# Optimization experiments

Hardware: AMD Instinct MI355X
Metric: run time of the kernel (lower is better)

The kernel has to match this reference:

```python
import jax, jax.numpy as jnp
import numpy as np
import math

NEG_BIG = -1e9

def setup_inputs() -> dict:
    key = jax.random.key(0)
    k1, k2, k3 = jax.random.split(key, 3)
    N, C, T = 16, 64, 2048
    qkv = jax.random.normal(k1, (N, 3 * C, T), dtype=jnp.float32)
    pos = jax.random.normal(k2, (N, C, T), dtype=jnp.float32)
    attn_mask = jax.random.randint(k3, (N, T, T), 0, 2) == 1  # bool mask, True = masked
    return {"qkv": qkv, "pos": pos, "attn_mask": attn_mask}

def reference(qkv, pos, attn_mask):
    ch = qkv.shape[1] // 3
    q, k, v = jnp.split(qkv, 3, axis=1)  # each [N, C, T]
    q = q + pos
    k = k + pos
    v = v + pos
    scale = 1.0 / math.sqrt(math.sqrt(ch))
    # [N, T, T] attention logits
    weight = jnp.einsum('bct,bcs->bts', q * scale, k * scale)
    weight = jnp.where(attn_mask, NEG_BIG, weight)
    weight = jax.nn.softmax(weight.astype(jnp.float32), axis=-1).astype(weight.dtype)
    return jnp.einsum('bts,bcs->bct', weight, v)
```

## Files before the change

### kernel.cpp

```cpp
#include <hip/hip_runtime.h>
#include <hip/hip_bf16.h>

typedef float f32x4 __attribute__((ext_vector_type(4)));
typedef unsigned int u32x4 __attribute__((ext_vector_type(4)));
typedef short s16x8 __attribute__((ext_vector_type(8)));

#define L2E 1.44269504088896340736f

static __device__ __forceinline__ unsigned int bf16_rne(float f) {
    unsigned int u = __builtin_bit_cast(unsigned int, f);
    return (u + 0x7fffu + ((u >> 16) & 1u)) >> 16;
}
static __device__ __forceinline__ unsigned int pack_bf16x2(float lo, float hi) {
    return bf16_rne(lo) | (bf16_rne(hi) << 16);
}
static __device__ __forceinline__ unsigned int cvt_pk_bf16(float lo, float hi) {
    unsigned int r;
    asm("v_cvt_pk_bf16_f32 %0, %1, %2" : "=v"(r) : "v"(lo), "v"(hi));
    return r;
}

__global__ __launch_bounds__(256) void qkv_prep(const float* __restrict__ qkv,
                                                const float* __restrict__ pos,
                                                unsigned short* __restrict__ qs,
                                                unsigned short* __restrict__ kt,
                                                unsigned short* __restrict__ vt)
{
    __shared__ unsigned short QtS[64][72];
    __shared__ unsigned short KtS[64][72];
    const int b    = blockIdx.y;
    const int t0   = blockIdx.x * 64;
    const int i    = threadIdx.x;
    const int crow = i >> 2;
    const int t16  = (i & 3) * 16;
    const float QSCALE = 0.125f * L2E;

    float pr[16];
    {
        const f32x4* pp = reinterpret_cast<const f32x4*>(
            pos + ((size_t)(b * 64 + crow)) * 2048 + t0 + t16);
        #pragma unroll
        for (int j = 0; j < 4; ++j) {
            f32x4 v = __builtin_nontemporal_load(pp + j);
            pr[4*j+0] = v[0]; pr[4*j+1] = v[1]; pr[4*j+2] = v[2]; pr[4*j+3] = v[3];
        }
    }
    const float* qp = qkv + ((size_t)(b * 192 + crow)) * 2048 + t0 + t16;
    {
        #pragma unroll
        for (int j = 0; j < 4; ++j) {
            f32x4 v = __builtin_nontemporal_load(reinterpret_cast<const f32x4*>(qp) + j);
            #pragma unroll
            for (int e = 0; e < 4; ++e)
                QtS[t16 + 4*j + e][crow] =
                    (unsigned short)bf16_rne((v[e] + pr[4*j+e]) * QSCALE);
        }
    }
    {
        const float* kp = qp + (size_t)64 * 2048;
        #pragma unroll
        for (int j = 0; j < 4; ++j) {
            f32x4 v = __builtin_nontemporal_load(reinterpret_cast<const f32x4*>(kp) + j);
            #pragma unroll
            for (int e = 0; e < 4; ++e)
                KtS[t16 + 4*j + e][crow] =
                    (unsigned short)bf16_rne(v[e] + pr[4*j+e]);
        }
    }
    {
        const float* vp = qp + (size_t)128 * 2048;
        unsigned int vv[8];
        #pragma unroll
        for (int j = 0; j < 4; ++j) {
            f32x4 v = __builtin_nontemporal_load(reinterpret_cast<const f32x4*>(vp) + j);
            vv[2*j+0] = pack_bf16x2(v[0] + pr[4*j+0], v[1] + pr[4*j+1]);
            vv[2*j+1] = pack_bf16x2(v[2] + pr[4*j+2], v[3] + pr[4*j+3]);
        }
        unsigned short* dst = vt + ((size_t)(b * 64 + crow)) * 2048 + t0 + t16;
        reinterpret_cast<u32x4*>(dst)[0] = (u32x4){vv[0], vv[1], vv[2], vv[3]};
        reinterpret_cast<u32x4*>(dst)[1] = (u32x4){vv[4], vv[5], vv[6], vv[7]};
    }
    __syncthreads();
    {
        const int trow = i >> 2;
        const int c16  = (i & 3) * 16;
        u32x4 a0 = *reinterpret_cast<const u32x4*>(&QtS[trow][c16]);
        u32x4 a1 = *reinterpret_cast<const u32x4*>(&QtS[trow][c16 + 8]);
        unsigned short* qd = qs + ((size_t)(b * 2048 + t0 + trow)) * 64 + c16;
        reinterpret_cast<u32x4*>(qd)[0] = a0;
        reinterpret_cast<u32x4*>(qd)[1] = a1;
        u32x4 b0 = *reinterpret_cast<const u32x4*>(&KtS[trow][c16]);
        u32x4 b1 = *reinterpret_cast<const u32x4*>(&KtS[trow][c16 + 8]);
        unsigned short* kd = kt + ((size_t)(b * 2048 + t0 + trow)) * 64 + c16;
        reinterpret_cast<u32x4*>(kd)[0] = b0;
        reinterpret_cast<u32x4*>(kd)[1] = b1;
    }
}

__global__ __launch_bounds__(256) void attn_kernel(const unsigned short* __restrict__ qs,
                                                   const unsigned short* __restrict__ kt,
                                                   const unsigned short* __restrict__ vt,
                                                   const void* __restrict__ maskp,
                                                   float* __restrict__ out)
{
    __shared__ unsigned short Klds[2][64][72];
    __shared__ unsigned short Vlds[2][64][72];

    const int b    = blockIdx.y;
    const int t0   = blockIdx.x * 64;
    const int tid  = threadIdx.x;
    const int wave = tid >> 6;
    const int lane = tid & 63;
    const int ln   = lane & 15;
    const int lg   = lane >> 4;

    unsigned int accm = 0;
    {
        const unsigned int* mu = (const unsigned int*)maskp;
        #pragma unroll
        for (int j = 0; j < 16; ++j) accm |= mu[j];
    }
    const bool maskIsBool = (accm & 0xffffff00u) != 0u;

    const int tg = t0 + 16 * wave + ln;
    s16x8 qf[2];
    #pragma unroll
    for (int kc = 0; kc < 2; ++kc)
        qf[kc] = *reinterpret_cast<const s16x8*>(
            qs + ((size_t)(b * 2048 + tg)) * 64 + 32 * kc + 8 * lg);

    f32x4 acc[4];
    #pragma unroll
    for (int n = 0; n < 4; ++n) acc[n] = (f32x4){0.f, 0.f, 0.f, 0.f};
    float M = -3.0e38f, L = 0.0f;

    const int stRow = tid >> 2;
    const int stC16 = (tid & 3) * 16;
    const unsigned short* kbase = kt + ((size_t)(b * 2048 + stRow)) * 64 + stC16;
    const unsigned short* vbase = vt + ((size_t)(b * 64 + stRow)) * 2048 + stC16;
    const size_t mrowoff = ((size_t)b * 2048 + (size_t)tg) * 2048;

    unsigned int m_cur[4];

    {
        u32x4 ka0 = reinterpret_cast<const u32x4*>(kbase)[0];
        u32x4 ka1 = reinterpret_cast<const u32x4*>(kbase)[1];
        u32x4 va0 = reinterpret_cast<const u32x4*>(vbase)[0];
        u32x4 va1 = reinterpret_cast<const u32x4*>(vbase)[1];
        if (maskIsBool) {
            const unsigned char* mp = (const unsigned char*)maskp + mrowoff + 4 * lg;
            #pragma unroll
            for (int ti = 0; ti < 4; ++ti)
                m_cur[ti] = __builtin_nontemporal_load(
                    reinterpret_cast<const unsigned int*>(mp + 16 * ti));
        } else {
            const u32x4* mp = reinterpret_cast<const u32x4*>(
                (const unsigned int*)maskp + mrowoff + 4 * lg);
            #pragma unroll
            for (int ti = 0; ti < 4; ++ti) {
                u32x4 x = __builtin_nontemporal_load(mp + 4 * ti);
                m_cur[ti] = (x[0] ? 1u : 0u) | ((x[1] ? 1u : 0u) << 8) |
                            ((x[2] ? 1u : 0u) << 16) | ((x[3] ? 1u : 0u) << 24);
            }
        }
        *reinterpret_cast<u32x4*>(&Klds[0][stRow][stC16])     = ka0;
        *reinterpret_cast<u32x4*>(&Klds[0][stRow][stC16 + 8]) = ka1;
        *reinterpret_cast<u32x4*>(&Vlds[0][stRow][stC16])     = va0;
        *reinterpret_cast<u32x4*>(&Vlds[0][stRow][stC16 + 8]) = va1;
    }
    __syncthreads();

    int cur = 0;
    for (int st = 0; st < 32; ++st) {
        u32x4 ka0, ka1, va0, va1;
        unsigned int m_nxt[4];
        const bool pf = (st < 31);
        if (pf) {
            const int s1 = (st + 1) * 64;
            const unsigned short* ks = kbase + (size_t)s1 * 64;
            const unsigned short* vs = vbase + s1;
            ka0 = reinterpret_cast<const u32x4*>(ks)[0];
            ka1 = reinterpret_cast<const u32x4*>(ks)[1];
            va0 = reinterpret_cast<const u32x4*>(vs)[0];
            va1 = reinterpret_cast<const u32x4*>(vs)[1];
            if (maskIsBool) {
                const unsigned char* mp = (const unsigned char*)maskp + mrowoff + s1 + 4 * lg;
                #pragma unroll
                for (int ti = 0; ti < 4; ++ti)
                    m_nxt[ti] = __builtin_nontemporal_load(
                        reinterpret_cast<const unsigned int*>(mp + 16 * ti));
            } else {
                const u32x4* mp = reinterpret_cast<const u32x4*>(
                    (const unsigned int*)maskp + mrowoff + s1 + 4 * lg);
                #pragma unroll
                for (int ti = 0; ti < 4; ++ti) {
                    u32x4 x = __builtin_nontemporal_load(mp + 4 * ti);
                    m_nxt[ti] = (x[0] ? 1u : 0u) | ((x[1] ? 1u : 0u) << 8) |
                                ((x[2] ? 1u : 0u) << 16) | ((x[3] ? 1u : 0u) << 24);
                }
            }
        }

        f32x4 S[4];
        #pragma unroll
        for (int ti = 0; ti < 4; ++ti) S[ti] = (f32x4){0.f, 0.f, 0.f, 0.f};
        __builtin_amdgcn_s_setprio(1);
        #pragma unroll
        for (int kc = 0; kc < 2; ++kc) {
            #pragma unroll
            for (int ti = 0; ti < 4; ++ti) {
                s16x8 kf = *reinterpret_cast<const s16x8*>(
                    &Klds[cur][16 * ti + ln][32 * kc + 8 * lg]);
                S[ti] = __builtin_amdgcn_mfma_f32_16x16x32_bf16(kf, qf[kc], S[ti], 0, 0, 0);
            }
        }
        __builtin_amdgcn_s_setprio(0);

        float p[4][4];
        #pragma unroll
        for (int ti = 0; ti < 4; ++ti) {
            #pragma unroll
            for (int r = 0; r < 4; ++r)
                p[ti][r] = ((m_cur[ti] >> (8 * r)) & 0xffu) ? -1e9f : S[ti][r];
        }
        float tm = fmaxf(fmaxf(fmaxf(p[0][0], p[0][1]), fmaxf(p[0][2], p[0][3])),
                         fmaxf(fmaxf(p[1][0], p[1][1]), fmaxf(p[1][2], p[1][3])));
        tm = fmaxf(tm, fmaxf(fmaxf(fmaxf(p[2][0], p[2][1]), fmaxf(p[2][2], p[2][3])),
                             fmaxf(fmaxf(p[3][0], p[3][1]), fmaxf(p[3][2], p[3][3]))));
        tm = fmaxf(tm, __shfl_xor(tm, 16, 64));
        tm = fmaxf(tm, __shfl_xor(tm, 32, 64));
        if (!__all(tm <= M)) {
            const float Mn    = fmaxf(M, tm);
            const float alpha = exp2f(M - Mn);
            L *= alpha;
            #pragma unroll
            for (int n = 0; n < 4; ++n) acc[n] *= alpha;
            M = Mn;
        }
        float tsum = 0.f;
        #pragma unroll
        for (int ti = 0; ti < 4; ++ti)
            #pragma unroll
            for (int r = 0; r < 4; ++r) {
                p[ti][r] = exp2f(p[ti][r] - M);
                tsum += p[ti][r];
            }
        tsum += __shfl_xor(tsum, 16, 64);
        tsum += __shfl_xor(tsum, 32, 64);
        L += tsum;

        unsigned int pk[4][2];
        #pragma unroll
        for (int ti = 0; ti < 4; ++ti) {
            pk[ti][0] = cvt_pk_bf16(p[ti][0], p[ti][1]);
            pk[ti][1] = cvt_pk_bf16(p[ti][2], p[ti][3]);
        }
        unsigned int pfr[2][4];
        #pragma unroll
        for (int kc2 = 0; kc2 < 2; ++kc2)
            #pragma unroll
            for (int a2 = 0; a2 < 2; ++a2)
                #pragma unroll
                for (int b2 = 0; b2 < 2; ++b2)
                    #pragma unroll
                    for (int e = 0; e < 2; ++e) {
                        int src = ln + 16 * (2 * (lg & 1) + e);
                        unsigned int v = (unsigned int)__shfl(
                            (int)pk[2 * kc2 + a2][b2], src, 64);
                        if ((lg >> 1) == a2) pfr[kc2][2 * e + b2] = v;
                    }

        __builtin_amdgcn_s_setprio(1);
        #pragma unroll
        for (int kc2 = 0; kc2 < 2; ++kc2) {
            union { unsigned int u[4]; s16x8 s; } pu;
            pu.u[0] = pfr[kc2][0]; pu.u[1] = pfr[kc2][1];
            pu.u[2] = pfr[kc2][2]; pu.u[3] = pfr[kc2][3];
            #pragma unroll
            for (int n = 0; n < 4; ++n) {
                s16x8 vf = *reinterpret_cast<const s16x8*>(
                    &Vlds[cur][16 * n + ln][32 * kc2 + 8 * lg]);
                acc[n] = __builtin_amdgcn_mfma_f32_16x16x32_bf16(vf, pu.s, acc[n], 0, 0, 0);
            }
        }
        __builtin_amdgcn_s_setprio(0);

        if (pf) {
            *reinterpret_cast<u32x4*>(&Klds[cur ^ 1][stRow][stC16])     = ka0;
            *reinterpret_cast<u32x4*>(&Klds[cur ^ 1][stRow][stC16 + 8]) = ka1;
            *reinterpret_cast<u32x4*>(&Vlds[cur ^ 1][stRow][stC16])     = va0;
            *reinterpret_cast<u32x4*>(&Vlds[cur ^ 1][stRow][stC16 + 8]) = va1;
            #pragma unroll
            for (int ti = 0; ti < 4; ++ti) m_cur[ti] = m_nxt[ti];
            __syncthreads();
            cur ^= 1;
        }
    }

    const float inv = 1.0f / L;
    #pragma unroll
    for (int n = 0; n < 4; ++n)
        #pragma unroll
        for (int r = 0; r < 4; ++r)
            __builtin_nontemporal_store(
                acc[n][r] * inv,
                &out[((size_t)(b * 64 + 16 * n + 4 * lg + r)) * 2048 + t0 + 16 * wave + ln]);
}

extern "C" void kernel_launch(void* const* d_in, const int* in_sizes, int n_in,
                              void* d_out, int out_size, void* d_ws, size_t ws_size,
                              hipStream_t stream) {
    const float* qkv = (const float*)d_in[0];
    const float* pos = (const float*)d_in[1];
    const void*  msk = d_in[2];
    float* outp = (float*)d_out;
    unsigned short* ws = (unsigned short*)d_ws;
    const size_t PLANE = (size_t)16 * 2048 * 64;
    unsigned short* qs = ws;
    unsigned short* kt = ws + PLANE;
    unsigned short* vt = ws + 2 * PLANE;

    dim3 grid(2048 / 64, 16);
    qkv_prep<<<grid, 256, 0, stream>>>(qkv, pos, qs, kt, vt);
    attn_kernel<<<grid, 256, 0, stream>>>(qs, kt, vt, msk, outp);
}
```

Baseline: 114.0 us.

## Pre-swizzle K/V into MFMA fragment layout and load directly from global

The prep kernel now writes K and V in the exact per-lane MFMA fragment order. The attention kernel therefore loads fragments straight from global/L2 into registers and drops the LDS staging and per-tile __syncthreads. The loop is double-buffered in registers, with the mask type handled through a template. A 1D grid reorders blocks so that batches are interleaved. This removes LDS traffic and barriers, but K/V tiles are now re-read from cache by each wave, and register pressure rises with launch_bounds(256,2).

```diff
diff --git a/kernel.cpp b/kernel.cpp
--- a/kernel.cpp
+++ b/kernel.cpp
@@ -23,8 +23,8 @@
 __global__ __launch_bounds__(256) void qkv_prep(const float* __restrict__ qkv,
                                                 const float* __restrict__ pos,
                                                 unsigned short* __restrict__ qs,
-                                                unsigned short* __restrict__ kt,
-                                                unsigned short* __restrict__ vt)
+                                                unsigned short* __restrict__ ktf,
+                                                unsigned short* __restrict__ vtf)
 {
     __shared__ unsigned short QtS[64][72];
     __shared__ unsigned short KtS[64][72];
@@ -76,9 +76,20 @@
             vv[2*j+0] = pack_bf16x2(v[0] + pr[4*j+0], v[1] + pr[4*j+1]);
             vv[2*j+1] = pack_bf16x2(v[2] + pr[4*j+2], v[3] + pr[4*j+3]);
         }
-        unsigned short* dst = vt + ((size_t)(b * 64 + crow)) * 2048 + t0 + t16;
-        reinterpret_cast<u32x4*>(dst)[0] = (u32x4){vv[0], vv[1], vv[2], vv[3]};
-        reinterpret_cast<u32x4*>(dst)[1] = (u32x4){vv[4], vv[5], vv[6], vv[7]};
+        const int n   = crow >> 4;
+        const int lnv = crow & 15;
+        const int sb  = t0 >> 6;
+        #pragma unroll
+        for (int h = 0; h < 2; ++h) {
+            const int soff = t16 + 8 * h;
+            const int kc2  = soff >> 5;
+            const int lgv  = (soff >> 3) & 3;
+            unsigned short* dst = vtf +
+                ((((size_t)(b * 32 + sb)) * 4 + n) * 2 + kc2) * 512 +
+                (lnv + 16 * lgv) * 8;
+            *reinterpret_cast<u32x4*>(dst) =
+                (u32x4){vv[4*h+0], vv[4*h+1], vv[4*h+2], vv[4*h+3]};
+        }
     }
     __syncthreads();
     {
@@ -89,40 +100,161 @@
         unsigned short* qd = qs + ((size_t)(b * 2048 + t0 + trow)) * 64 + c16;
         reinterpret_cast<u32x4*>(qd)[0] = a0;
         reinterpret_cast<u32x4*>(qd)[1] = a1;
-        u32x4 b0 = *reinterpret_cast<const u32x4*>(&KtS[trow][c16]);
-        u32x4 b1 = *reinterpret_cast<const u32x4*>(&KtS[trow][c16 + 8]);
-        unsigned short* kd = kt + ((size_t)(b * 2048 + t0 + trow)) * 64 + c16;
-        reinterpret_cast<u32x4*>(kd)[0] = b0;
-        reinterpret_cast<u32x4*>(kd)[1] = b1;
-    }
-}
-
-__global__ __launch_bounds__(256) void attn_kernel(const unsigned short* __restrict__ qs,
-                                                   const unsigned short* __restrict__ kt,
-                                                   const unsigned short* __restrict__ vt,
-                                                   const void* __restrict__ maskp,
-                                                   float* __restrict__ out)
-{
-    __shared__ unsigned short Klds[2][64][72];
-    __shared__ unsigned short Vlds[2][64][72];
-
-    const int b    = blockIdx.y;
-    const int t0   = blockIdx.x * 64;
-    const int tid  = threadIdx.x;
+    }
+    {
+        const int g   = i >> 6;
+        const int l   = i & 63;
+        const int lnk = l & 15;
+        const int lgk = l >> 4;
+        #pragma unroll
+        for (int kc = 0; kc < 2; ++kc) {
+            u32x4 d = *reinterpret_cast<const u32x4*>(
+                &KtS[16 * g + lnk][32 * kc + 8 * lgk]);
+            unsigned short* dst = ktf +
+                (((size_t)(b * 128 + (t0 >> 4) + g)) * 2 + kc) * 512 + l * 8;
+            *reinterpret_cast<u32x4*>(dst) = d;
+        }
+    }
+}
+
+__device__ __forceinline__ void load_kfrag(s16x8 (&kf)[2][4],
+        const unsigned short* __restrict__ ktf, size_t bk, int lane, int st)
+{
+    #pragma unroll
+    for (int kc = 0; kc < 2; ++kc)
+        #pragma unroll
+        for (int ti = 0; ti < 4; ++ti)
+            kf[kc][ti] = *reinterpret_cast<const s16x8*>(
+                ktf + ((bk + 4 * st + ti) * 2 + kc) * 512 + lane * 8);
+}
+
+template<bool MB>
+__device__ __forceinline__ void load_mask(unsigned int (&mf)[4],
+        const void* __restrict__ maskp, size_t mrowoff, int lg, int st)
+{
+    if (MB) {
+        const unsigned char* mp = (const unsigned char*)maskp + mrowoff + st * 64 + 4 * lg;
+        #pragma unroll
+        for (int ti = 0; ti < 4; ++ti)
+            mf[ti] = __builtin_nontemporal_load(
+                reinterpret_cast<const unsigned int*>(mp + 16 * ti));
+    } else {
+        const unsigned int* mp = (const unsigned int*)maskp + mrowoff + st * 64 + 4 * lg;
+        #pragma unroll
+        for (int ti = 0; ti < 4; ++ti) {
+            u32x4 x = __builtin_nontemporal_load(
+                reinterpret_cast<const u32x4*>(mp + 16 * ti));
+            mf[ti] = (x[0] ? 1u : 0u) | ((x[1] ? 1u : 0u) << 8) |
+                     ((x[2] ? 1u : 0u) << 16) | ((x[3] ? 1u : 0u) << 24);
+        }
+    }
+}
+
+__device__ __forceinline__ void attn_body(
+        const s16x8 (&kf)[2][4], const unsigned int (&mf)[4],
+        const s16x8 (&qf)[2], f32x4 (&acc)[4], float& M, float& L,
+        const unsigned short* __restrict__ vtf, size_t bv,
+        int lane, int ln, int lg, int st)
+{
+    s16x8 vf[2][4];
+    #pragma unroll
+    for (int kc2 = 0; kc2 < 2; ++kc2)
+        #pragma unroll
+        for (int n = 0; n < 4; ++n)
+            vf[kc2][n] = *reinterpret_cast<const s16x8*>(
+                vtf + (((bv + st) * 4 + n) * 2 + kc2) * 512 + lane * 8);
+
+    f32x4 S[4];
+    #pragma unroll
+    for (int ti = 0; ti < 4; ++ti) S[ti] = (f32x4){0.f, 0.f, 0.f, 0.f};
+    __builtin_amdgcn_s_setprio(1);
+    #pragma unroll
+    for (int kc = 0; kc < 2; ++kc)
+        #pragma unroll
+        for (int ti = 0; ti < 4; ++ti)
+            S[ti] = __builtin_amdgcn_mfma_f32_16x16x32_bf16(kf[kc][ti], qf[kc], S[ti], 0, 0, 0);
+    __builtin_amdgcn_s_setprio(0);
+
+    float p[4][4];
+    #pragma unroll
+    for (int ti = 0; ti < 4; ++ti)
+        #pragma unroll
+        for (int r = 0; r < 4; ++r)
+            p[ti][r] = ((mf[ti] >> (8 * r)) & 0xffu) ? -1e9f : S[ti][r];
+    float tm = fmaxf(fmaxf(fmaxf(p[0][0], p[0][1]), fmaxf(p[0][2], p[0][3])),
+                     fmaxf(fmaxf(p[1][0], p[1][1]), fmaxf(p[1][2], p[1][3])));
+    tm = fmaxf(tm, fmaxf(fmaxf(fmaxf(p[2][0], p[2][1]), fmaxf(p[2][2], p[2][3])),
+                         fmaxf(fmaxf(p[3][0], p[3][1]), fmaxf(p[3][2], p[3][3]))));
+    tm = fmaxf(tm, __shfl_xor(tm, 16, 64));
+    tm = fmaxf(tm, __shfl_xor(tm, 32, 64));
+    if (!__all(tm <= M)) {
+        const float Mn    = fmaxf(M, tm);
+        const float alpha = exp2f(M - Mn);
+        L *= alpha;
+        #pragma unroll
+        for (int n = 0; n < 4; ++n) acc[n] *= alpha;
+        M = Mn;
+    }
+    float tsum = 0.f;
+    #pragma unroll
+    for (int ti = 0; ti < 4; ++ti)
+        #pragma unroll
+        for (int r = 0; r < 4; ++r) {
+            p[ti][r] = exp2f(p[ti][r] - M);
+            tsum += p[ti][r];
+        }
+    tsum += __shfl_xor(tsum, 16, 64);
+    tsum += __shfl_xor(tsum, 32, 64);
+    L += tsum;
+
+    unsigned int pk[4][2];
+    #pragma unroll
+    for (int ti = 0; ti < 4; ++ti) {
+        pk[ti][0] = cvt_pk_bf16(p[ti][0], p[ti][1]);
+        pk[ti][1] = cvt_pk_bf16(p[ti][2], p[ti][3]);
+    }
+    unsigned int pfr[2][4];
+    #pragma unroll
+    for (int kc2 = 0; kc2 < 2; ++kc2)
+        #pragma unroll
+        for (int a2 = 0; a2 < 2; ++a2)
+            #pragma unroll
+            for (int b2 = 0; b2 < 2; ++b2)
+                #pragma unroll
+                for (int e = 0; e < 2; ++e) {
+                    int src = ln + 16 * (2 * (lg & 1) + e);
+                    unsigned int v = (unsigned int)__shfl(
+                        (int)pk[2 * kc2 + a2][b2], src, 64);
+                    if ((lg >> 1) == a2) pfr[kc2][2 * e + b2] = v;
+                }
+
+    __builtin_amdgcn_s_setprio(1);
+    #pragma unroll
+    for (int kc2 = 0; kc2 < 2; ++kc2) {
+        union { unsigned int u[4]; s16x8 s; } pu;
+        pu.u[0] = pfr[kc2][0]; pu.u[1] = pfr[kc2][1];
+        pu.u[2] = pfr[kc2][2]; pu.u[3] = pfr[kc2][3];
+        #pragma unroll
+        for (int n = 0; n < 4; ++n)
+            acc[n] = __builtin_amdgcn_mfma_f32_16x16x32_bf16(vf[kc2][n], pu.s, acc[n], 0, 0, 0);
+    }
+    __builtin_amdgcn_s_setprio(0);
+}
+
+template<bool MB>
+__device__ __forceinline__ void attn_run(
+        const unsigned short* __restrict__ qs,
+        const unsigned short* __restrict__ ktf,
+        const unsigned short* __restrict__ vtf,
+        const void* __restrict__ maskp,
+        float* __restrict__ out, int b, int t0, int tid)
+{
     const int wave = tid >> 6;
     const int lane = tid & 63;
     const int ln   = lane & 15;
     const int lg   = lane >> 4;
-
-    unsigned int accm = 0;
-    {
-        const unsigned int* mu = (const unsigned int*)maskp;
-        #pragma unroll
-        for (int j = 0; j < 16; ++j) accm |= mu[j];
-    }
-    const bool maskIsBool = (accm & 0xffffff00u) != 0u;
-
-    const int tg = t0 + 16 * wave + ln;
+    const int tg   = t0 + 16 * wave + ln;
+
     s16x8 qf[2];
     #pragma unroll
     for (int kc = 0; kc < 2; ++kc)
@@ -134,167 +266,25 @@
     for (int n = 0; n < 4; ++n) acc[n] = (f32x4){0.f, 0.f, 0.f, 0.f};
     float M = -3.0e38f, L = 0.0f;
 
-    const int stRow = tid >> 2;
-    const int stC16 = (tid & 3) * 16;
-    const unsigned short* kbase = kt + ((size_t)(b * 2048 + stRow)) * 64 + stC16;
-    const unsigned short* vbase = vt + ((size_t)(b * 64 + stRow)) * 2048 + stC16;
+    const size_t bk = (size_t)b * 128;
+    const size_t bv = (size_t)b * 32;
     const size_t mrowoff = ((size_t)b * 2048 + (size_t)tg) * 2048;
 
-    unsigned int m_cur[4];
-
-    {
-        u32x4 ka0 = reinterpret_cast<const u32x4*>(kbase)[0];
-        u32x4 ka1 = reinterpret_cast<const u32x4*>(kbase)[1];
-        u32x4 va0 = reinterpret_cast<const u32x4*>(vbase)[0];
-        u32x4 va1 = reinterpret_cast<const u32x4*>(vbase)[1];
-        if (maskIsBool) {
-            const unsigned char* mp = (const unsigned char*)maskp + mrowoff + 4 * lg;
-            #pragma unroll
-            for (int ti = 0; ti < 4; ++ti)
-                m_cur[ti] = __builtin_nontemporal_load(
-                    reinterpret_cast<const unsigned int*>(mp + 16 * ti));
-        } else {
-            const u32x4* mp = reinterpret_cast<const u32x4*>(
-                (const unsigned int*)maskp + mrowoff + 4 * lg);
-            #pragma unroll
-            for (int ti = 0; ti < 4; ++ti) {
-                u32x4 x = __builtin_nontemporal_load(mp + 4 * ti);
-                m_cur[ti] = (x[0] ? 1u : 0u) | ((x[1] ? 1u : 0u) << 8) |
-                            ((x[2] ? 1u : 0u) << 16) | ((x[3] ? 1u : 0u) << 24);
-            }
-        }
-        *reinterpret_cast<u32x4*>(&Klds[0][stRow][stC16])     = ka0;
-        *reinterpret_cast<u32x4*>(&Klds[0][stRow][stC16 + 8]) = ka1;
-        *reinterpret_cast<u32x4*>(&Vlds[0][stRow][stC16])     = va0;
-        *reinterpret_cast<u32x4*>(&Vlds[0][stRow][stC16 + 8]) = va1;
-    }
-    __syncthreads();
-
-    int cur = 0;
-    for (int st = 0; st < 32; ++st) {
-        u32x4 ka0, ka1, va0, va1;
-        unsigned int m_nxt[4];
-        const bool pf = (st < 31);
-        if (pf) {
-            const int s1 = (st + 1) * 64;
-            const unsigned short* ks = kbase + (size_t)s1 * 64;
-            const unsigned short* vs = vbase + s1;
-            ka0 = reinterpret_cast<const u32x4*>(ks)[0];
-            ka1 = reinterpret_cast<const u32x4*>(ks)[1];
-            va0 = reinterpret_cast<const u32x4*>(vs)[0];
-            va1 = reinterpret_cast<const u32x4*>(vs)[1];
-            if (maskIsBool) {
-                const unsigned char* mp = (const unsigned char*)maskp + mrowoff + s1 + 4 * lg;
-                #pragma unroll
-                for (int ti = 0; ti < 4; ++ti)
-                    m_nxt[ti] = __builtin_nontemporal_load(
-                        reinterpret_cast<const unsigned int*>(mp + 16 * ti));
-            } else {
-                const u32x4* mp = reinterpret_cast<const u32x4*>(
-                    (const unsigned int*)maskp + mrowoff + s1 + 4 * lg);
-                #pragma unroll
-                for (int ti = 0; ti < 4; ++ti) {
-                    u32x4 x = __builtin_nontemporal_load(mp + 4 * ti);
-                    m_nxt[ti] = (x[0] ? 1u : 0u) | ((x[1] ? 1u : 0u) << 8) |
-                                ((x[2] ? 1u : 0u) << 16) | ((x[3] ? 1u : 0u) << 24);
-                }
-            }
-        }
-
-        f32x4 S[4];
-        #pragma unroll
-        for (int ti = 0; ti < 4; ++ti) S[ti] = (f32x4){0.f, 0.f, 0.f, 0.f};
-        __builtin_amdgcn_s_setprio(1);
-        #pragma unroll
-        for (int kc = 0; kc < 2; ++kc) {
-            #pragma unroll
-            for (int ti = 0; ti < 4; ++ti) {
-                s16x8 kf = *reinterpret_cast<const s16x8*>(
-                    &Klds[cur][16 * ti + ln][32 * kc + 8 * lg]);
-                S[ti] = __builtin_amdgcn_mfma_f32_16x16x32_bf16(kf, qf[kc], S[ti], 0, 0, 0);
-            }
-        }
-        __builtin_amdgcn_s_setprio(0);
-
-        float p[4][4];
-        #pragma unroll
-        for (int ti = 0; ti < 4; ++ti) {
-            #pragma unroll
-            for (int r = 0; r < 4; ++r)
-                p[ti][r] = ((m_cur[ti] >> (8 * r)) & 0xffu) ? -1e9f : S[ti][r];
-        }
-        float tm = fmaxf(fmaxf(fmaxf(p[0][0], p[0][1]), fmaxf(p[0][2], p[0][3])),
-                         fmaxf(fmaxf(p[1][0], p[1][1]), fmaxf(p[1][2], p[1][3])));
-        tm = fmaxf(tm, fmaxf(fmaxf(fmaxf(p[2][0], p[2][1]), fmaxf(p[2][2], p[2][3])),
-                             fmaxf(fmaxf(p[3][0], p[3][1]), fmaxf(p[3][2], p[3][3]))));
-        tm = fmaxf(tm, __shfl_xor(tm, 16, 64));
-        tm = fmaxf(tm, __shfl_xor(tm, 32, 64));
-        if (!__all(tm <= M)) {
-            const float Mn    = fmaxf(M, tm);
-            const float alpha = exp2f(M - Mn);
-            L *= alpha;
-            #pragma unroll
-            for (int n = 0; n < 4; ++n) acc[n] *= alpha;
-            M = Mn;
-        }
-        float tsum = 0.f;
-        #pragma unroll
-        for (int ti = 0; ti < 4; ++ti)
-            #pragma unroll
-            for (int r = 0; r < 4; ++r) {
-                p[ti][r] = exp2f(p[ti][r] - M);
-                tsum += p[ti][r];
-            }
-        tsum += __shfl_xor(tsum, 16, 64);
-        tsum += __shfl_xor(tsum, 32, 64);
-        L += tsum;
-
-        unsigned int pk[4][2];
-        #pragma unroll
-        for (int ti = 0; ti < 4; ++ti) {
-            pk[ti][0] = cvt_pk_bf16(p[ti][0], p[ti][1]);
-            pk[ti][1] = cvt_pk_bf16(p[ti][2], p[ti][3]);
-        }
-        unsigned int pfr[2][4];
-        #pragma unroll
-        for (int kc2 = 0; kc2 < 2; ++kc2)
-            #pragma unroll
-            for (int a2 = 0; a2 < 2; ++a2)
-                #pragma unroll
-                for (int b2 = 0; b2 < 2; ++b2)
-                    #pragma unroll
-                    for (int e = 0; e < 2; ++e) {
-                        int src = ln + 16 * (2 * (lg & 1) + e);
-                        unsigned int v = (unsigned int)__shfl(
-                            (int)pk[2 * kc2 + a2][b2], src, 64);
-                        if ((lg >> 1) == a2) pfr[kc2][2 * e + b2] = v;
-                    }
-
-        __builtin_amdgcn_s_setprio(1);
-        #pragma unroll
-        for (int kc2 = 0; kc2 < 2; ++kc2) {
-            union { unsigned int u[4]; s16x8 s; } pu;
-            pu.u[0] = pfr[kc2][0]; pu.u[1] = pfr[kc2][1];
-            pu.u[2] = pfr[kc2][2]; pu.u[3] = pfr[kc2][3];
-            #pragma unroll
-            for (int n = 0; n < 4; ++n) {
-                s16x8 vf = *reinterpret_cast<const s16x8*>(
-                    &Vlds[cur][16 * n + ln][32 * kc2 + 8 * lg]);
-                acc[n] = __builtin_amdgcn_mfma_f32_16x16x32_bf16(vf, pu.s, acc[n], 0, 0, 0);
-            }
-        }
-        __builtin_amdgcn_s_setprio(0);
-
-        if (pf) {
-            *reinterpret_cast<u32x4*>(&Klds[cur ^ 1][stRow][stC16])     = ka0;
-            *reinterpret_cast<u32x4*>(&Klds[cur ^ 1][stRow][stC16 + 8]) = ka1;
-            *reinterpret_cast<u32x4*>(&Vlds[cur ^ 1][stRow][stC16])     = va0;
-            *reinterpret_cast<u32x4*>(&Vlds[cur ^ 1][stRow][stC16 + 8]) = va1;
-            #pragma unroll
-            for (int ti = 0; ti < 4; ++ti) m_cur[ti] = m_nxt[ti];
-            __syncthreads();
-            cur ^= 1;
-        }
+    s16x8 fka[2][4], fkb[2][4];
+    unsigned int fm0[4], fm1[4];
+    load_kfrag(fka, ktf, bk, lane, 0);
+    load_mask<MB>(fm0, maskp, mrowoff, lg, 0);
+
+    #pragma unroll 1
+    for (int sb = 0; sb < 32; sb += 2) {
+        load_kfrag(fkb, ktf, bk, lane, sb + 1);
+        load_mask<MB>(fm1, maskp, mrowoff, lg, sb + 1);
+        attn_body(fka, fm0, qf, acc, M, L, vtf, bv, lane, ln, lg, sb);
+        if (sb + 2 < 32) {
+            load_kfrag(fka, ktf, bk, lane, sb + 2);
+            load_mask<MB>(fm0, maskp, mrowoff, lg, sb + 2);
+        }
+        attn_body(fkb, fm1, qf, acc, M, L, vtf, bv, lane, ln, lg, sb + 1);
     }
 
     const float inv = 1.0f / L;
@@ -304,7 +294,30 @@
         for (int r = 0; r < 4; ++r)
             __builtin_nontemporal_store(
                 acc[n][r] * inv,
-                &out[((size_t)(b * 64 + 16 * n + 4 * lg + r)) * 2048 + t0 + 16 * wave + ln]);
+                &out[((size_t)(b * 64 + 16 * n + 4 * lg + r)) * 2048 + tg]);
+}
+
+__global__ __launch_bounds__(256, 2) void attn_kernel(
+        const unsigned short* __restrict__ qs,
+        const unsigned short* __restrict__ ktf,
+        const unsigned short* __restrict__ vtf,
+        const void* __restrict__ maskp,
+        float* __restrict__ out)
+{
+    const int id = blockIdx.x;
+    const int b  = (id & 7) + 8 * ((id >> 3) & 1);
+    const int t0 = (id >> 4) * 64;
+
+    unsigned int accm = 0;
+    {
+        const unsigned int* mu = (const unsigned int*)maskp;
+        #pragma unroll
+        for (int j = 0; j < 16; ++j) accm |= mu[j];
+    }
+    if ((accm & 0xffffff00u) != 0u)
+        attn_run<true >(qs, ktf, vtf, maskp, out, b, t0, threadIdx.x);
+    else
+        attn_run<false>(qs, ktf, vtf, maskp, out, b, t0, threadIdx.x);
 }
 
 extern "C" void kernel_launch(void* const* d_in, const int* in_sizes, int n_in,
@@ -316,11 +329,11 @@
     float* outp = (float*)d_out;
     unsigned short* ws = (unsigned short*)d_ws;
     const size_t PLANE = (size_t)16 * 2048 * 64;
-    unsigned short* qs = ws;
-    unsigned short* kt = ws + PLANE;
-    unsigned short* vt = ws + 2 * PLANE;
-
-    dim3 grid(2048 / 64, 16);
-    qkv_prep<<<grid, 256, 0, stream>>>(qkv, pos, qs, kt, vt);
-    attn_kernel<<<grid, 256, 0, stream>>>(qs, kt, vt, msk, outp);
-}
+    unsigned short* qs  = ws;
+    unsigned short* ktf = ws + PLANE;
+    unsigned short* vtf = ws + 2 * PLANE;
+
+    dim3 pgrid(2048 / 64, 16);
+    qkv_prep<<<pgrid, 256, 0, stream>>>(qkv, pos, qs, ktf, vtf);
+    attn_kernel<<<512, 256, 0, stream>>>(qs, ktf, vtf, msk, outp);
+}
```

Result: slower. 133.0 us (+16.7%).
